# Kernel optimization log

Hardware: AMD Instinct MI355X
Metric: run time of the kernel (lower is better)

The kernel has to match this reference:

```python
import jax, jax.numpy as jnp
import numpy as np

B, G, N_IN, N_HID, N_OUT = 2, 4096, 8, 32, 32
ALPHA, BETA, BN_EPS = 0.005, 5e-5, 1e-5
EDGE_P = 0.05  # adjacency density


def _lin_init(k, fan_in, fan_out):
    k1, k2 = jax.random.split(k)
    lim = 1.0 / np.sqrt(fan_in)
    W = jax.random.uniform(k1, (fan_in, fan_out), minval=-lim, maxval=lim, dtype=jnp.float32)
    b = jax.random.uniform(k2, (fan_out,), minval=-lim, maxval=lim, dtype=jnp.float32)
    return W, b


def setup_inputs() -> dict:
    key = jax.random.key(0)
    ks = jax.random.split(key, 12)
    W_infer, b_infer = _lin_init(ks[0], N_IN, N_HID)
    W_e1, b_e1 = _lin_init(ks[1], 2 * N_HID, 1)
    W_e2, b_e2 = _lin_init(ks[2], 2 * N_HID, 1)
    W_n1, b_n1 = _lin_init(ks[3], 2 * N_HID, N_OUT)
    W_n2, b_n2 = _lin_init(ks[4], 2 * N_HID, N_OUT)
    W_m1, b_m1 = _lin_init(ks[5], 2 * N_HID, N_OUT)
    W_m2, b_m2 = _lin_init(ks[6], 2 * N_HID, N_OUT)
    x = jax.random.normal(ks[7], (B, G, N_IN), dtype=jnp.float32)
    edges1 = jax.random.bernoulli(ks[8], EDGE_P, (G, G)).astype(jnp.float32)
    edges2 = jax.random.bernoulli(ks[9], EDGE_P, (G, G)).astype(jnp.float32)
    bn_gamma = jnp.ones((G,), jnp.float32)
    bn_beta = jnp.zeros((G,), jnp.float32)
    return dict(x=x, edges1=edges1, edges2=edges2, W_infer=W_infer, b_infer=b_infer,
                W_e1=W_e1, b_e1=b_e1, W_e2=W_e2, b_e2=b_e2,
                W_n1=W_n1, b_n1=b_n1, W_n2=W_n2, b_n2=b_n2,
                W_m1=W_m1, b_m1=b_m1, W_m2=W_m2, b_m2=b_m2,
                bn_gamma=bn_gamma, bn_beta=bn_beta)


def _mp_block(x, adj, coef, W_e, b_e, W_n, b_n, W_m, b_m):
    # x: [B,G,H]. Torch builds edge feature at flat index k=i*G+j as cat([x_j, x_i])
    # (shape2 = col gather, shape1 = row gather). We keep the same math without
    # materializing the [B,G*G,2H] tensor.
    Hh = x.shape[-1]
    s_src = x @ W_e[:Hh]   # [B,G,1]  (x_j part of mlp_edge)
    s_dst = x @ W_e[Hh:]   # [B,G,1]  (x_i part of mlp_edge)
    logits = s_dst[:, :, None, 0] + s_src[:, None, :, 0] + b_e[0]   # [B,G,G] at (i,j)
    w = adj + coef * (adj == 0).astype(x.dtype)                     # ori_edge + coef*thres_edge
    e = jax.nn.sigmoid(logits) * w[None]                            # [B,G,G]
    # receive at node i: sum_j e_ij * [x_j, x_i]
    recv_src = jnp.einsum('bij,bjh->bih', e, x)                     # sum_j e_ij x_j
    recv_dst = x * jnp.sum(e, axis=2)[..., None]                    # x_i * sum_j e_ij
    recv = jnp.concatenate([recv_src, recv_dst], axis=-1)           # [B,G,2H]
    recv = jax.nn.elu(recv @ W_n + b_n)                             # nodes_mlp + elu
    upd = jnp.concatenate([recv, x], axis=-1) @ W_m + b_m           # mesg_merge (mode='cat')
    return jax.nn.elu(upd)


def _forward(x, edges1, edges2, W_infer, b_infer, W_e1, b_e1, W_e2, b_e2,
             W_n1, b_n1, W_n2, b_n2, W_m1, b_m1, W_m2, b_m2, bn_gamma, bn_beta):
    h = jax.nn.elu(x @ W_infer + b_infer)                           # infer + elu, [B,G,H]
    h = _mp_block(h, edges1, ALPHA, W_e1, b_e1, W_n1, b_n1, W_m1, b_m1)
    # BatchNorm1d(gene_num) on [B, G, n_out]: per-gene stats over (batch, feature)
    mu = jnp.mean(h, axis=(0, 2), keepdims=True)
    var = jnp.var(h, axis=(0, 2), keepdims=True)
    h = (h - mu) * jax.lax.rsqrt(var + BN_EPS)
    h = h * bn_gamma[None, :, None] + bn_beta[None, :, None]
    return _mp_block(h, edges2, BETA, W_e2, b_e2, W_n2, b_n2, W_m2, b_m2)


def reference(x, edges1, edges2, W_infer, b_infer, W_e1, b_e1, W_e2, b_e2,
              W_n1, b_n1, W_n2, b_n2, W_m1, b_m1, W_m2, b_m2, bn_gamma, bn_beta):
    return _forward(x, edges1, edges2, W_infer, b_infer, W_e1, b_e1, W_e2, b_e2,
                    W_n1, b_n1, W_n2, b_n2, W_m1, b_m1, W_m2, b_m2, bn_gamma, bn_beta)
```

## Files before the change

### kernel.cpp

```cpp
#include <hip/hip_runtime.h>

#define G 4096
#define BSZ 2
#define NIN 8
#define HID 32
#define NLOG2E (-1.4426950408889634f)

typedef __attribute__((ext_vector_type(8))) short short8;
typedef __attribute__((ext_vector_type(4))) float floatx4;
typedef unsigned short ushort_t;
typedef unsigned int uint_t;

__device__ __forceinline__ float elu1(float v) {
    return v > 0.f ? v : (__expf(v) - 1.f);
}
__device__ __forceinline__ ushort_t f2bf(float f) {
    unsigned u = __float_as_uint(f);
    u += 0x7fffu + ((u >> 16) & 1u);
    return (ushort_t)(u >> 16);
}

__global__ __launch_bounds__(256) void k_setup1(
    const float* __restrict__ x, const float* __restrict__ W,
    const float* __restrict__ bias, const float* __restrict__ We,
    float* __restrict__ h0, ushort_t* __restrict__ hTb,
    float* __restrict__ ssrc, float* __restrict__ sdst) {
    __shared__ __align__(16) ushort_t hs[HID][264];
    int tid = threadIdx.x;
    int t = blockIdx.x * 256 + tid;
    int b = t >> 12;
    int g0 = (blockIdx.x & 15) * 256;
    float xin[NIN];
    const float* xp = x + t * NIN;
#pragma unroll
    for (int k = 0; k < NIN; k++) xin[k] = xp[k];
    float ss = 0.f, sd = 0.f;
    float* hp = h0 + (size_t)t * HID;
#pragma unroll
    for (int o = 0; o < HID; o++) {
        float v = bias[o];
#pragma unroll
        for (int k = 0; k < NIN; k++) v += xin[k] * W[k * HID + o];
        v = elu1(v);
        hp[o] = v;
        hs[o][tid] = f2bf(v);
        ss += v * We[o];
        sd += v * We[HID + o];
    }
    ssrc[t] = ss;
    sdst[t] = sd;
    __syncthreads();
#pragma unroll
    for (int p = 0; p < 4; p++) {
        int row = p * 8 + (tid >> 5);
        int c = (tid & 31) * 8;
        short8 v8 = *(const short8*)&hs[row][c];
        *(short8*)(void*)&hTb[(size_t)(b * HID + row) * G + g0 + c] = v8;
    }
}

template <bool DO_BN>
__global__ __launch_bounds__(1024, 4) void k_fused(
    const float* __restrict__ adj, const float* __restrict__ ssrc,
    const float* __restrict__ sdst, const ushort_t* __restrict__ hTb_in,
    const float* __restrict__ bep, float coef, const float* __restrict__ hin,
    const float* __restrict__ Wn, const float* __restrict__ bnb,
    const float* __restrict__ Wm, const float* __restrict__ bmb,
    const float* __restrict__ gamma, const float* __restrict__ beta,
    const float* __restrict__ We2, float* __restrict__ outp,
    ushort_t* __restrict__ hTb_out, float* __restrict__ s2s,
    float* __restrict__ s2d) {
    union SMemU {
        float ssm[BSZ][G];
        struct {
            float rec[32][68];
            float rec2[32][68];
            float esg[16][2];
            ushort_t tb[BSZ][HID][16];
        } p;
    };
    __shared__ __align__(16) SMemU sm;
    __shared__ __align__(16) uint_t abits[128][16];
    __shared__ __align__(16) float red[14][64][9];
    __shared__ __align__(16) float Wns[2048];
    __shared__ __align__(16) float Wms[2048];

    int tid = threadIdx.x;
    int g0 = blockIdx.x * 16;
    int l = tid & 63, w = tid >> 6;
    int b = w >> 3, jq = w & 7;

    if (tid < 512) {
        ((float4*)Wns)[tid] = ((const float4*)Wn)[tid];
    } else {
        int t2 = tid - 512;
        ((float4*)Wms)[t2] = ((const float4*)Wm)[t2];
    }
#pragma unroll
    for (int r = 0; r < 2; r++) {
        int idx = r * 4096 + tid * 4;
        int bb = idx >> 12, j = idx & 4095;
        float4 s4 = *(const float4*)&ssrc[bb * G + j];
        s4.x *= NLOG2E; s4.y *= NLOG2E; s4.z *= NLOG2E; s4.w *= NLOG2E;
        *(float4*)&sm.ssm[bb][j] = s4;
    }
    {
        int jw = tid >> 3;
        bool st = (tid & 7) == 0;
        int sh = (tid & 7) * 4;
#pragma unroll
        for (int s = 0; s < 16; s++) {
            float4 v4 = *(const float4*)&adj[(size_t)(g0 + s) * G + tid * 4];
            uint_t nib = (uint_t)(v4.x != 0.f) | ((uint_t)(v4.y != 0.f) << 1) |
                         ((uint_t)(v4.z != 0.f) << 2) | ((uint_t)(v4.w != 0.f) << 3);
            uint_t wd = nib << sh;
            wd |= __shfl_xor(wd, 1);
            wd |= __shfl_xor(wd, 2);
            wd |= __shfl_xor(wd, 4);
            if (st) abits[jw][s] = wd;
        }
    }

    int m = l & 15, kg = l >> 4;
    float sd2 = (sdst[b * G + g0 + m] + bep[0]) * NLOG2E;
    float wm1 = 1.f - coef;
    int jstart = jq * 512;
    const ushort_t* hb0 = hTb_in + (size_t)(b * HID + m) * G + jstart + kg * 8;
    const ushort_t* hb1 = hb0 + (size_t)16 * G;
    floatx4 c0 = {0.f, 0.f, 0.f, 0.f}, c1 = {0.f, 0.f, 0.f, 0.f};
    float es = 0.f;
    short8 pb0[2], pb1[2];
#pragma unroll
    for (int d = 0; d < 2; d++) {
        pb0[d] = *(const short8*)(const void*)(hb0 + d * 32);
        pb1[d] = *(const short8*)(const void*)(hb1 + d * 32);
    }
    __syncthreads();
    const float* svp = &sm.ssm[b][jstart + kg * 8];
    const uint_t* abp = &abits[jq * 16][m];

#pragma unroll 4
    for (int jc = 0; jc < 16; jc++) {
        int cur = jc & 1;
        short8 bf0 = pb0[cur], bf1 = pb1[cur];
        if (jc + 2 < 16) {
            int o = (jc + 2) * 32;
            pb0[cur] = *(const short8*)(const void*)(hb0 + o);
            pb1[cur] = *(const short8*)(const void*)(hb1 + o);
        }
        uint_t bw = abp[jc * 16];
        float4 s0 = *(const float4*)&svp[jc * 32];
        float4 s1 = *(const float4*)&svp[jc * 32 + 4];
        float sv[8] = {s0.x, s0.y, s0.z, s0.w, s1.x, s1.y, s1.z, s1.w};
        short8 af;
#pragma unroll
        for (int t = 0; t < 8; t++) {
            float bitf = (float)((bw >> (kg * 8 + t)) & 1u);
            float wgt = __builtin_fmaf(bitf, wm1, coef);
            float ex = exp2f(sd2 + sv[t]);
            float e = __builtin_amdgcn_rcpf(1.f + ex) * wgt;
            es += e;
            af[t] = (short)f2bf(e);
        }
        c0 = __builtin_amdgcn_mfma_f32_16x16x32_bf16(af, bf0, c0, 0, 0, 0);
        c1 = __builtin_amdgcn_mfma_f32_16x16x32_bf16(af, bf1, c1, 0, 0, 0);
    }
    if (jq) {
        int widx = b * 7 + jq - 1;
#pragma unroll
        for (int r = 0; r < 4; r++) {
            red[widx][l][r] = c0[r];
            red[widx][l][4 + r] = c1[r];
        }
        red[widx][l][8] = es;
    }
    __syncthreads();
    if (!jq) {
#pragma unroll
        for (int q = 0; q < 7; q++) {
            int widx = b * 7 + q;
#pragma unroll
            for (int r = 0; r < 4; r++) {
                c0[r] += red[widx][l][r];
                c1[r] += red[widx][l][4 + r];
            }
            es += red[widx][l][8];
        }
        es += __shfl_xor(es, 16);
        es += __shfl_xor(es, 32);
#pragma unroll
        for (int r = 0; r < 4; r++) {
            int gene = (l >> 4) * 4 + r;
            sm.p.rec[gene * 2 + b][m] = c0[r];
            sm.p.rec[gene * 2 + b][16 + m] = c1[r];
        }
        if (l < 16) sm.p.esg[l][b] = es;
    }
    __syncthreads();

    int rl = tid >> 5, hh = tid & 31;
    int gene = rl >> 1, bb = rl & 1;
    float xv = hin[((size_t)(bb * G + g0 + gene)) * HID + hh];
    sm.p.rec[rl][32 + hh] = xv * sm.p.esg[gene][bb];
    __syncthreads();

    float v = bnb[hh];
#pragma unroll
    for (int k4 = 0; k4 < 16; k4++) {
        float4 r4 = *(const float4*)&sm.p.rec[rl][k4 * 4];
        v += r4.x * Wns[(k4 * 4 + 0) * HID + hh];
        v += r4.y * Wns[(k4 * 4 + 1) * HID + hh];
        v += r4.z * Wns[(k4 * 4 + 2) * HID + hh];
        v += r4.w * Wns[(k4 * 4 + 3) * HID + hh];
    }
    v = elu1(v);
    sm.p.rec2[rl][hh] = v;
    sm.p.rec2[rl][32 + hh] = xv;
    float u = bmb[hh];
#pragma unroll
    for (int k4 = 0; k4 < 16; k4++) {
        float4 r4 = *(const float4*)&sm.p.rec2[rl][k4 * 4];
        u += r4.x * Wms[(k4 * 4 + 0) * HID + hh];
        u += r4.y * Wms[(k4 * 4 + 1) * HID + hh];
        u += r4.z * Wms[(k4 * 4 + 2) * HID + hh];
        u += r4.w * Wms[(k4 * 4 + 3) * HID + hh];
    }
    float h1v = elu1(u);
    if (!DO_BN) {
        outp[((size_t)(bb * G + g0 + gene)) * HID + hh] = h1v;
    } else {
        float s = h1v, sq = h1v * h1v;
#pragma unroll
        for (int mm = 32; mm; mm >>= 1) {
            s += __shfl_xor(s, mm);
            sq += __shfl_xor(sq, mm);
        }
        float mu = s * (1.f / 64.f);
        float var = sq * (1.f / 64.f) - mu * mu;
        float rstd = rsqrtf(var + 1e-5f);
        float hn = (h1v - mu) * rstd * gamma[g0 + gene] + beta[g0 + gene];
        outp[((size_t)(bb * G + g0 + gene)) * HID + hh] = hn;
        sm.p.tb[bb][hh][gene] = f2bf(hn);
        float ps = hn * We2[hh], pd = hn * We2[HID + hh];
#pragma unroll
        for (int mm = 16; mm; mm >>= 1) {
            ps += __shfl_xor(ps, mm);
            pd += __shfl_xor(pd, mm);
        }
        if (hh == 0) {
            s2s[bb * G + g0 + gene] = ps;
            s2d[bb * G + g0 + gene] = pd;
        }
        __syncthreads();
        if (tid < 128) {
            int b2 = tid >> 6, c = (tid >> 1) & 31, half = tid & 1;
            short8 v8 = *(const short8*)&sm.p.tb[b2][c][half * 8];
            *(short8*)(void*)&hTb_out[(size_t)(b2 * HID + c) * G + g0 + half * 8] = v8;
        }
    }
}

extern "C" void kernel_launch(void* const* d_in, const int* in_sizes, int n_in,
                              void* d_out, int out_size, void* d_ws, size_t ws_size,
                              hipStream_t stream) {
    const float* x      = (const float*)d_in[0];
    const float* edges1 = (const float*)d_in[1];
    const float* edges2 = (const float*)d_in[2];
    const float* W_inf  = (const float*)d_in[3];
    const float* b_inf  = (const float*)d_in[4];
    const float* W_e1   = (const float*)d_in[5];
    const float* b_e1   = (const float*)d_in[6];
    const float* W_e2   = (const float*)d_in[7];
    const float* b_e2   = (const float*)d_in[8];
    const float* W_n1   = (const float*)d_in[9];
    const float* b_n1   = (const float*)d_in[10];
    const float* W_n2   = (const float*)d_in[11];
    const float* b_n2   = (const float*)d_in[12];
    const float* W_m1   = (const float*)d_in[13];
    const float* b_m1   = (const float*)d_in[14];
    const float* W_m2   = (const float*)d_in[15];
    const float* b_m2   = (const float*)d_in[16];
    const float* bn_g   = (const float*)d_in[17];
    const float* bn_b   = (const float*)d_in[18];
    float* out = (float*)d_out;

    float* ws = (float*)d_ws;
    float* h0   = ws;
    float* h1n  = ws + 262144;
    float* s1s  = ws + 524288;
    float* s1d  = ws + 532480;
    float* s2s  = ws + 540672;
    float* s2d  = ws + 548864;
    ushort_t* hTb  = (ushort_t*)(ws + 557056);
    ushort_t* hTb2 = (ushort_t*)(ws + 688128);

    const float ALPHA = 0.005f, BETA = 5e-5f;

    k_setup1<<<32, 256, 0, stream>>>(x, W_inf, b_inf, W_e1, h0, hTb, s1s, s1d);
    k_fused<true><<<G / 16, 1024, 0, stream>>>(
        edges1, s1s, s1d, hTb, b_e1, ALPHA, h0, W_n1, b_n1, W_m1, b_m1,
        bn_g, bn_b, W_e2, h1n, hTb2, s2s, s2d);
    k_fused<false><<<G / 16, 1024, 0, stream>>>(
        edges2, s2s, s2d, hTb2, b_e2, BETA, h1n, W_n2, b_n2, W_m2, b_m2,
        nullptr, nullptr, nullptr, out, nullptr, nullptr, nullptr);
}
```

Measured before the change: 237.2 us.

## Stream adjacency and source scores from global memory instead of LDS staging

Drops the up-front shared-memory staging of the scaled source scores and the packed adjacency bitmask. Each lane now prefetches its adjacency floats directly into registers, double-buffered alongside the bf16 features, and reads source scores straight from global memory. The log2e scaling moves into the kernels that produce the scores. This removes a large LDS buffer, one barrier and the bit-packing shuffles, which should help occupancy and shorten the prologue. In exchange, each block reads adjacency in uncoalesced-ish 32-byte pieces, and both batch halves reload the same adjacency rows, leaning more on L2.

Result: slower. 258.9 us (+9.2%).

```diff
diff --git a/kernel.cpp b/kernel.cpp
--- a/kernel.cpp
+++ b/kernel.cpp
@@ -47,8 +47,8 @@
         ss += v * We[o];
         sd += v * We[HID + o];
     }
-    ssrc[t] = ss;
-    sdst[t] = sd;
+    ssrc[t] = ss * NLOG2E;
+    sdst[t] = sd * NLOG2E;
     __syncthreads();
 #pragma unroll
     for (int p = 0; p < 4; p++) {
@@ -70,18 +70,11 @@
     const float* __restrict__ We2, float* __restrict__ outp,
     ushort_t* __restrict__ hTb_out, float* __restrict__ s2s,
     float* __restrict__ s2d) {
-    union SMemU {
-        float ssm[BSZ][G];
-        struct {
-            float rec[32][68];
-            float rec2[32][68];
-            float esg[16][2];
-            ushort_t tb[BSZ][HID][16];
-        } p;
-    };
-    __shared__ __align__(16) SMemU sm;
-    __shared__ __align__(16) uint_t abits[128][16];
     __shared__ __align__(16) float red[14][64][9];
+    __shared__ __align__(16) float rec[32][68];
+    __shared__ __align__(16) float rec2[32][68];
+    __shared__ __align__(16) float esg[16][2];
+    __shared__ __align__(16) ushort_t tbuf[BSZ][HID][16];
     __shared__ __align__(16) float Wns[2048];
     __shared__ __align__(16) float Wms[2048];
 
@@ -96,67 +89,47 @@
         int t2 = tid - 512;
         ((float4*)Wms)[t2] = ((const float4*)Wm)[t2];
     }
-#pragma unroll
-    for (int r = 0; r < 2; r++) {
-        int idx = r * 4096 + tid * 4;
-        int bb = idx >> 12, j = idx & 4095;
-        float4 s4 = *(const float4*)&ssrc[bb * G + j];
-        s4.x *= NLOG2E; s4.y *= NLOG2E; s4.z *= NLOG2E; s4.w *= NLOG2E;
-        *(float4*)&sm.ssm[bb][j] = s4;
-    }
-    {
-        int jw = tid >> 3;
-        bool st = (tid & 7) == 0;
-        int sh = (tid & 7) * 4;
-#pragma unroll
-        for (int s = 0; s < 16; s++) {
-            float4 v4 = *(const float4*)&adj[(size_t)(g0 + s) * G + tid * 4];
-            uint_t nib = (uint_t)(v4.x != 0.f) | ((uint_t)(v4.y != 0.f) << 1) |
-                         ((uint_t)(v4.z != 0.f) << 2) | ((uint_t)(v4.w != 0.f) << 3);
-            uint_t wd = nib << sh;
-            wd |= __shfl_xor(wd, 1);
-            wd |= __shfl_xor(wd, 2);
-            wd |= __shfl_xor(wd, 4);
-            if (st) abits[jw][s] = wd;
-        }
-    }
 
     int m = l & 15, kg = l >> 4;
-    float sd2 = (sdst[b * G + g0 + m] + bep[0]) * NLOG2E;
-    float wm1 = 1.f - coef;
+    float sd2 = sdst[b * G + g0 + m] + bep[0] * NLOG2E;
     int jstart = jq * 512;
     const ushort_t* hb0 = hTb_in + (size_t)(b * HID + m) * G + jstart + kg * 8;
     const ushort_t* hb1 = hb0 + (size_t)16 * G;
+    const float* ap = adj + (size_t)(g0 + m) * G + jstart + kg * 8;
+    const float* sp = ssrc + b * G + jstart + kg * 8;
     floatx4 c0 = {0.f, 0.f, 0.f, 0.f}, c1 = {0.f, 0.f, 0.f, 0.f};
     float es = 0.f;
     short8 pb0[2], pb1[2];
+    float4 av0[2], av1[2];
 #pragma unroll
     for (int d = 0; d < 2; d++) {
         pb0[d] = *(const short8*)(const void*)(hb0 + d * 32);
         pb1[d] = *(const short8*)(const void*)(hb1 + d * 32);
-    }
-    __syncthreads();
-    const float* svp = &sm.ssm[b][jstart + kg * 8];
-    const uint_t* abp = &abits[jq * 16][m];
+        av0[d] = *(const float4*)(ap + d * 32);
+        av1[d] = *(const float4*)(ap + d * 32 + 4);
+    }
 
 #pragma unroll 4
     for (int jc = 0; jc < 16; jc++) {
         int cur = jc & 1;
         short8 bf0 = pb0[cur], bf1 = pb1[cur];
+        float4 a0 = av0[cur], a1 = av1[cur];
         if (jc + 2 < 16) {
             int o = (jc + 2) * 32;
             pb0[cur] = *(const short8*)(const void*)(hb0 + o);
             pb1[cur] = *(const short8*)(const void*)(hb1 + o);
-        }
-        uint_t bw = abp[jc * 16];
-        float4 s0 = *(const float4*)&svp[jc * 32];
-        float4 s1 = *(const float4*)&svp[jc * 32 + 4];
+            av0[cur] = *(const float4*)(ap + o);
+            av1[cur] = *(const float4*)(ap + o + 4);
+        }
+        float4 s0 = *(const float4*)(sp + jc * 32);
+        float4 s1 = *(const float4*)(sp + jc * 32 + 4);
         float sv[8] = {s0.x, s0.y, s0.z, s0.w, s1.x, s1.y, s1.z, s1.w};
+        float avf[8] = {a0.x, a0.y, a0.z, a0.w, a1.x, a1.y, a1.z, a1.w};
         short8 af;
 #pragma unroll
         for (int t = 0; t < 8; t++) {
-            float bitf = (float)((bw >> (kg * 8 + t)) & 1u);
-            float wgt = __builtin_fmaf(bitf, wm1, coef);
+            float v = avf[t];
+            float wgt = (v != 0.f) ? v : coef;
             float ex = exp2f(sd2 + sv[t]);
             float e = __builtin_amdgcn_rcpf(1.f + ex) * wgt;
             es += e;
@@ -191,35 +164,35 @@
 #pragma unroll
         for (int r = 0; r < 4; r++) {
             int gene = (l >> 4) * 4 + r;
-            sm.p.rec[gene * 2 + b][m] = c0[r];
-            sm.p.rec[gene * 2 + b][16 + m] = c1[r];
-        }
-        if (l < 16) sm.p.esg[l][b] = es;
+            rec[gene * 2 + b][m] = c0[r];
+            rec[gene * 2 + b][16 + m] = c1[r];
+        }
+        if (l < 16) esg[l][b] = es;
     }
     __syncthreads();
 
     int rl = tid >> 5, hh = tid & 31;
     int gene = rl >> 1, bb = rl & 1;
     float xv = hin[((size_t)(bb * G + g0 + gene)) * HID + hh];
-    sm.p.rec[rl][32 + hh] = xv * sm.p.esg[gene][bb];
+    rec[rl][32 + hh] = xv * esg[gene][bb];
     __syncthreads();
 
     float v = bnb[hh];
 #pragma unroll
     for (int k4 = 0; k4 < 16; k4++) {
-        float4 r4 = *(const float4*)&sm.p.rec[rl][k4 * 4];
+        float4 r4 = *(const float4*)&rec[rl][k4 * 4];
         v += r4.x * Wns[(k4 * 4 + 0) * HID + hh];
         v += r4.y * Wns[(k4 * 4 + 1) * HID + hh];
         v += r4.z * Wns[(k4 * 4 + 2) * HID + hh];
         v += r4.w * Wns[(k4 * 4 + 3) * HID + hh];
     }
     v = elu1(v);
-    sm.p.rec2[rl][hh] = v;
-    sm.p.rec2[rl][32 + hh] = xv;
+    rec2[rl][hh] = v;
+    rec2[rl][32 + hh] = xv;
     float u = bmb[hh];
 #pragma unroll
     for (int k4 = 0; k4 < 16; k4++) {
-        float4 r4 = *(const float4*)&sm.p.rec2[rl][k4 * 4];
+        float4 r4 = *(const float4*)&rec2[rl][k4 * 4];
         u += r4.x * Wms[(k4 * 4 + 0) * HID + hh];
         u += r4.y * Wms[(k4 * 4 + 1) * HID + hh];
         u += r4.z * Wms[(k4 * 4 + 2) * HID + hh];
@@ -240,7 +213,7 @@
         float rstd = rsqrtf(var + 1e-5f);
         float hn = (h1v - mu) * rstd * gamma[g0 + gene] + beta[g0 + gene];
         outp[((size_t)(bb * G + g0 + gene)) * HID + hh] = hn;
-        sm.p.tb[bb][hh][gene] = f2bf(hn);
+        tbuf[bb][hh][gene] = f2bf(hn);
         float ps = hn * We2[hh], pd = hn * We2[HID + hh];
 #pragma unroll
         for (int mm = 16; mm; mm >>= 1) {
@@ -248,13 +221,13 @@
             pd += __shfl_xor(pd, mm);
         }
         if (hh == 0) {
-            s2s[bb * G + g0 + gene] = ps;
-            s2d[bb * G + g0 + gene] = pd;
+            s2s[bb * G + g0 + gene] = ps * NLOG2E;
+            s2d[bb * G + g0 + gene] = pd * NLOG2E;
         }
         __syncthreads();
         if (tid < 128) {
             int b2 = tid >> 6, c = (tid >> 1) & 31, half = tid & 1;
-            short8 v8 = *(const short8*)&sm.p.tb[b2][c][half * 8];
+            short8 v8 = *(const short8*)&tbuf[b2][c][half * 8];
             *(short8*)(void*)&hTb_out[(size_t)(b2 * HID + c) * G + g0 + half * 8] = v8;
         }
     }
```

## Deepen prefetch of B operands and LDS scores, batch adjacency loads, prescale scores

Applied to the files above, without the earlier changes.

Folds the -log2(e) scaling of the source/destination scores into the kernels that produce them, so the fused kernel copies them straight into LDS. Issues the hTb global prefetch before the adjacency bit-packing and deepens it to four stages. The adjacency rows are loaded eight at a time before packing so more loads are in flight at once. Inside the main loop the LDS score and bit-mask reads are software-pipelined two iterations ahead and the loop is fully unrolled. All of this raises register use under a 1024-thread launch bound, which risks spills or lower occupancy.

Result: no change. 239.8 us (+1.1%).

```diff
diff --git a/kernel.cpp b/kernel.cpp
--- a/kernel.cpp
+++ b/kernel.cpp
@@ -47,8 +47,8 @@
         ss += v * We[o];
         sd += v * We[HID + o];
     }
-    ssrc[t] = ss;
-    sdst[t] = sd;
+    ssrc[t] = ss * NLOG2E;
+    sdst[t] = sd * NLOG2E;
     __syncthreads();
 #pragma unroll
     for (int p = 0; p < 4; p++) {
@@ -100,71 +100,91 @@
     for (int r = 0; r < 2; r++) {
         int idx = r * 4096 + tid * 4;
         int bb = idx >> 12, j = idx & 4095;
-        float4 s4 = *(const float4*)&ssrc[bb * G + j];
-        s4.x *= NLOG2E; s4.y *= NLOG2E; s4.z *= NLOG2E; s4.w *= NLOG2E;
-        *(float4*)&sm.ssm[bb][j] = s4;
-    }
+        *(float4*)&sm.ssm[bb][j] = *(const float4*)&ssrc[bb * G + j];
+    }
+
+    int m = l & 15, kg = l >> 4;
+    int jstart = jq * 512;
+    const ushort_t* hb0 = hTb_in + (size_t)(b * HID + m) * G + jstart + kg * 8;
+    const ushort_t* hb1 = hb0 + (size_t)16 * G;
+    short8 pb0[4], pb1[4];
+#pragma unroll
+    for (int d = 0; d < 4; d++) {
+        pb0[d] = *(const short8*)(const void*)(hb0 + d * 32);
+        pb1[d] = *(const short8*)(const void*)(hb1 + d * 32);
+    }
+
     {
         int jw = tid >> 3;
         bool st = (tid & 7) == 0;
-        int sh = (tid & 7) * 4;
-#pragma unroll
-        for (int s = 0; s < 16; s++) {
-            float4 v4 = *(const float4*)&adj[(size_t)(g0 + s) * G + tid * 4];
-            uint_t nib = (uint_t)(v4.x != 0.f) | ((uint_t)(v4.y != 0.f) << 1) |
-                         ((uint_t)(v4.z != 0.f) << 2) | ((uint_t)(v4.w != 0.f) << 3);
-            uint_t wd = nib << sh;
-            wd |= __shfl_xor(wd, 1);
-            wd |= __shfl_xor(wd, 2);
-            wd |= __shfl_xor(wd, 4);
-            if (st) abits[jw][s] = wd;
-        }
-    }
-
-    int m = l & 15, kg = l >> 4;
-    float sd2 = (sdst[b * G + g0 + m] + bep[0]) * NLOG2E;
-    float wm1 = 1.f - coef;
-    int jstart = jq * 512;
-    const ushort_t* hb0 = hTb_in + (size_t)(b * HID + m) * G + jstart + kg * 8;
-    const ushort_t* hb1 = hb0 + (size_t)16 * G;
+        int sh2 = (tid & 7) * 4;
+        float4 ld[8];
+#pragma unroll
+        for (int h = 0; h < 2; h++) {
+#pragma unroll
+            for (int s = 0; s < 8; s++)
+                ld[s] = *(const float4*)&adj[(size_t)(g0 + h * 8 + s) * G + tid * 4];
+#pragma unroll
+            for (int s = 0; s < 8; s++) {
+                float4 v4 = ld[s];
+                uint_t nib = (uint_t)(v4.x != 0.f) | ((uint_t)(v4.y != 0.f) << 1) |
+                             ((uint_t)(v4.z != 0.f) << 2) | ((uint_t)(v4.w != 0.f) << 3);
+                uint_t wd = nib << sh2;
+                wd |= __shfl_xor(wd, 1);
+                wd |= __shfl_xor(wd, 2);
+                wd |= __shfl_xor(wd, 4);
+                if (st) abits[jw][h * 8 + s] = wd;
+            }
+        }
+    }
+
+    float sd2 = sdst[b * G + g0 + m] + bep[0] * NLOG2E;
+    const float wm1 = 1.f - coef;
     floatx4 c0 = {0.f, 0.f, 0.f, 0.f}, c1 = {0.f, 0.f, 0.f, 0.f};
     float es = 0.f;
-    short8 pb0[2], pb1[2];
-#pragma unroll
-    for (int d = 0; d < 2; d++) {
-        pb0[d] = *(const short8*)(const void*)(hb0 + d * 32);
-        pb1[d] = *(const short8*)(const void*)(hb1 + d * 32);
-    }
-    __syncthreads();
+    __syncthreads();
+
     const float* svp = &sm.ssm[b][jstart + kg * 8];
     const uint_t* abp = &abits[jq * 16][m];
-
-#pragma unroll 4
+    float4 sv0[2], sv1[2];
+    uint_t bwr[2];
+#pragma unroll
+    for (int d = 0; d < 2; d++) {
+        sv0[d] = *(const float4*)&svp[d * 32];
+        sv1[d] = *(const float4*)&svp[d * 32 + 4];
+        bwr[d] = abp[d * 16];
+    }
+
+#pragma unroll
     for (int jc = 0; jc < 16; jc++) {
-        int cur = jc & 1;
-        short8 bf0 = pb0[cur], bf1 = pb1[cur];
+        int pc = jc & 3, lc = jc & 1;
+        short8 bf0 = pb0[pc], bf1 = pb1[pc];
+        float4 s0 = sv0[lc], s1 = sv1[lc];
+        uint_t bw = bwr[lc];
+        if (jc + 4 < 16) {
+            pb0[pc] = *(const short8*)(const void*)(hb0 + (jc + 4) * 32);
+            pb1[pc] = *(const short8*)(const void*)(hb1 + (jc + 4) * 32);
+        }
         if (jc + 2 < 16) {
-            int o = (jc + 2) * 32;
-            pb0[cur] = *(const short8*)(const void*)(hb0 + o);
-            pb1[cur] = *(const short8*)(const void*)(hb1 + o);
-        }
-        uint_t bw = abp[jc * 16];
-        float4 s0 = *(const float4*)&svp[jc * 32];
-        float4 s1 = *(const float4*)&svp[jc * 32 + 4];
+            sv0[lc] = *(const float4*)&svp[(jc + 2) * 32];
+            sv1[lc] = *(const float4*)&svp[(jc + 2) * 32 + 4];
+            bwr[lc] = abp[(jc + 2) * 16];
+        }
         float sv[8] = {s0.x, s0.y, s0.z, s0.w, s1.x, s1.y, s1.z, s1.w};
         short8 af;
 #pragma unroll
-        for (int t = 0; t < 8; t++) {
-            float bitf = (float)((bw >> (kg * 8 + t)) & 1u);
+        for (int t8 = 0; t8 < 8; t8++) {
+            float bitf = (float)((bw >> (kg * 8 + t8)) & 1u);
             float wgt = __builtin_fmaf(bitf, wm1, coef);
-            float ex = exp2f(sd2 + sv[t]);
+            float ex = exp2f(sd2 + sv[t8]);
             float e = __builtin_amdgcn_rcpf(1.f + ex) * wgt;
             es += e;
-            af[t] = (short)f2bf(e);
+            af[t8] = (short)f2bf(e);
         }
         c0 = __builtin_amdgcn_mfma_f32_16x16x32_bf16(af, bf0, c0, 0, 0, 0);
         c1 = __builtin_amdgcn_mfma_f32_16x16x32_bf16(af, bf1, c1, 0, 0, 0);
     }
+
     if (jq) {
         int widx = b * 7 + jq - 1;
 #pragma unroll
@@ -248,8 +268,8 @@
             pd += __shfl_xor(pd, mm);
         }
         if (hh == 0) {
-            s2s[bb * G + g0 + gene] = ps;
-            s2d[bb * G + g0 + gene] = pd;
+            s2s[bb * G + g0 + gene] = ps * NLOG2E;
+            s2d[bb * G + g0 + gene] = pd * NLOG2E;
         }
         __syncthreads();
         if (tid < 128) {
```
